# Kernel optimization log

Measured on AMD Instinct MI355X. Metric: run time of the kernel, lower is better.

## Reference

```python
import jax, jax.numpy as jnp
import numpy as np

B, N, P_CTR, K = 16, 2048, 256, 32
H, W = 24, 80
INFEA = 64
MLP = [64, 128, 128, 256]
DIST = 0.5
EPS = 1e-5


def setup_inputs() -> dict:
    key = jax.random.key(0)
    ks = jax.random.split(key, 12)
    inp = {}
    inp['pc'] = jax.random.normal(ks[0], (B, 3, N), jnp.float32)
    inp['feat'] = jax.random.normal(ks[1], (B, INFEA, N), jnp.float32)
    inp['img1'] = jax.random.normal(ks[2], (B, MLP[0], H, W), jnp.float32)
    inp['img2'] = jax.random.normal(ks[3], (B, MLP[1], H, W), jnp.float32)
    inp['P'] = jax.random.normal(ks[4], (B, 3, 4), jnp.float32)
    inp['query_v1'] = jax.random.randint(ks[5], (B, N), 0, H * W, dtype=jnp.int32)
    inp['new_pc'] = jax.random.normal(ks[6], (B, 3, P_CTR), jnp.float32)
    dims = [INFEA + 3] + MLP  # conv chain: 67->64->128->128->256, 1x1 convs, no bias
    for i in range(4):
        fan_in = dims[i]
        inp[f'w{i+1}'] = jax.random.normal(ks[7 + i], (dims[i + 1], dims[i]), jnp.float32) * np.sqrt(2.0 / fan_in)
        inp[f'g{i+1}'] = jnp.ones((dims[i + 1],), jnp.float32)   # BN gamma, init 1
        inp[f'b{i+1}'] = jnp.zeros((dims[i + 1],), jnp.float32)  # BN beta, init 0
    return inp


def query_depth_point(pc, new_pc, dist, k):
    # depth (z-axis) ball query: pc (B,3,N), new_pc (B,3,P) -> idx (B,P,k) int32, num (B,P)
    dz = jnp.abs(pc[:, 2, None, :] - new_pc[:, 2, :, None])  # (B,P,N)
    mask = dz < dist
    num = jnp.sum(mask, axis=-1).astype(jnp.int32)           # neighbor count per center
    # stable argsort of ~mask puts valid indices first, in ascending original order
    order = jnp.argsort(jnp.logical_not(mask), axis=-1, stable=True)
    idx = order[..., :k]
    slot_valid = jnp.arange(k)[None, None, :] < jnp.minimum(num, k)[..., None]
    idx = jnp.where(slot_valid, idx, idx[..., :1])           # pad with first valid index
    return idx.astype(jnp.int32), num


def gather_ch(x, idx):
    # x (B,C,M), idx (B,L) -> (B,C,L)
    return jnp.take_along_axis(x, idx[:, None, :], axis=2)


def conv_bn_relu(x, w, g, b):
    # 1x1 conv (no bias) + BatchNorm2d (training-mode batch stats) + ReLU
    y = jnp.einsum('oc,bcnk->bonk', w, x)
    m = jnp.mean(y, axis=(0, 2, 3), keepdims=True)
    v = jnp.var(y, axis=(0, 2, 3), keepdims=True)
    y = (y - m) * jax.lax.rsqrt(v + EPS)
    y = y * g[None, :, None, None] + b[None, :, None, None]
    return jax.nn.relu(y)


def reference(pc, feat, img1, img2, P, query_v1, new_pc,
              w1, g1, b1, w2, g2, b2, w3, g3, b3, w4, g4, b4):
    idx, num = query_depth_point(pc, new_pc, DIST, K)       # (B,P,K), (B,P)
    idx_flat = idx.reshape(B, P_CTR * K)
    idx_rgb = jnp.take_along_axis(query_v1, idx_flat, axis=1)  # (B,P*K) pixel ids

    grouped_pc = gather_ch(pc, idx_flat).reshape(B, 3, P_CTR, K) - new_pc[:, :, :, None]
    grouped_feat = gather_ch(feat, idx_flat).reshape(B, INFEA, P_CTR, K)
    rgb1 = gather_ch(img1.reshape(B, MLP[0], H * W), idx_rgb).reshape(B, MLP[0], P_CTR, K)
    rgb2 = gather_ch(img2.reshape(B, MLP[1], H * W), idx_rgb).reshape(B, MLP[1], P_CTR, K)

    grouped = jnp.concatenate([grouped_pc, grouped_feat], axis=1)  # (B,67,P,K)
    pf = conv_bn_relu(grouped, w1, g1, b1)                         # (B,64,P,K)
    f1 = jnp.concatenate([pf, rgb1], axis=1)                       # (B,128,P,K)
    pf = conv_bn_relu(pf, w2, g2, b2)                              # (B,128,P,K)
    f2 = jnp.concatenate([pf, rgb2], axis=1)                       # (B,256,P,K)
    pf = conv_bn_relu(pf, w3, g3, b3)
    pf = conv_bn_relu(pf, w4, g4, b4)                              # (B,256,P,K)
    out = jnp.concatenate([f1, f2, pf], axis=1)                    # (B,640,P,K)
    valid = (num > 0).reshape(B, 1, P_CTR, 1).astype(out.dtype)
    return out * valid
```

## Files before the change

kernel.cpp:

```cpp
#include <hip/hip_runtime.h>
#include <hip/hip_fp16.h>

#define BB 16
#define NN 2048
#define PC 256
#define KK 32
#define HWS 1920
#define PT (BB*PC*KK)
#define EPSF 1e-5f
#define THR 512

#define CH_IDXR 256
#define CH_IDX  257
#define CH_VAL  258
#define CH_FT   356
#define STATS_OFF ((size_t)259 << 13)

typedef _Float16 f16x8 __attribute__((ext_vector_type(8)));
typedef float    f32x4 __attribute__((ext_vector_type(4)));

__device__ __forceinline__ unsigned packh2(float lo, float hi) {
  unsigned a = (unsigned)__half_as_ushort(__float2half(lo));
  unsigned b = (unsigned)__half_as_ushort(__float2half(hi));
  return a | (b << 16);
}
__device__ __forceinline__ float h2lo(unsigned u) {
  return __half2float(__ushort_as_half((unsigned short)(u & 0xffffu)));
}
__device__ __forceinline__ float h2hi(unsigned u) {
  return __half2float(__ushort_as_half((unsigned short)(u >> 16)));
}

__global__ __launch_bounds__(256,2) void k_prep(
    const float* __restrict__ feat, float* out)
{
  __shared__ float tile[64][261];
  int tid = threadIdx.x;
  int b = blockIdx.x >> 3, n0 = (blockIdx.x & 7) << 8;
  #pragma unroll 8
  for (int c = 0; c < 64; c++)
    tile[c][tid] = feat[((size_t)b*64 + c)*NN + n0 + tid];
  __syncthreads();
  unsigned* ftw = (unsigned*)out + (((size_t)b*640 + CH_FT)<<13);
  #pragma unroll
  for (int e = tid; e < 256*32; e += 256) {
    int q = e & 31, nl = e >> 5;
    ftw[(size_t)(n0 + nl)*32 + q] = packh2(tile[2*q][nl], tile[2*q+1][nl]);
  }
}

template<bool WSC>
__global__ __launch_bounds__(256) void k_idx(
    const float* __restrict__ pc, const float* __restrict__ npc,
    const int* __restrict__ qv1, float* out, int* __restrict__ wsi)
{
  __shared__ int slots[4][KK];
  int tid = threadIdx.x;
  if (blockIdx.x < 5) {
    int i = blockIdx.x*256 + tid;
    if (i < 1152) out[STATS_OFF + i] = 0.0f;
  }
  int wl = tid >> 6, lane = tid & 63;
  int w = blockIdx.x*4 + wl;
  int b = w >> 8, p = w & 255;
  if (lane == 0) slots[wl][0] = 0;
  float zc = npc[(b*3+2)*PC + p];
  const float* pz = pc + ((size_t)b*3+2)*NN;
  int num = 0;
  for (int ci=0; ci<NN/64; ci++) {
    int n = ci*64 + lane;
    bool m = fabsf(pz[n] - zc) < 0.5f;
    unsigned long long mk = __ballot(m);
    if (m) {
      int rank = num + __popcll(mk & ((1ull<<lane)-1ull));
      if (rank < KK) slots[wl][rank] = n;
    }
    num += __popcll(mk);
  }
  __syncthreads();
  if (lane < KK) {
    int nj = (lane < num) ? slots[wl][lane] : slots[wl][0];
    size_t col = (size_t)p*KK + lane;
    int enc = (num > 0) ? qv1[b*NN + nj] : -1;
    ((int*)out)[(((size_t)b*640 + CH_IDX )<<13) + col] = nj;
    ((int*)out)[(((size_t)b*640 + CH_IDXR)<<13) + col] = enc;
    if constexpr (WSC) wsi[(size_t)b*8192 + col] = enc;
  }
  if (lane == 0)
    out[(((size_t)b*640 + CH_VAL)<<13) + (size_t)p*KK] = (num > 0) ? 1.0f : 0.0f;
}

template<int CIN, int CINP, int COUT, int BOCH, int WVP, int WVO, int WFP, int WFO,
         int XMODE, int XBASE, int YMODE, int YBASE, int STIN, int STOUT,
         int SWZ, int QR, int PFB, int TILES>
__global__ __launch_bounds__(THR,4) void k_mfma(
    const float* __restrict__ pc, const float* __restrict__ npc,
    const float* __restrict__ W,
    const float* __restrict__ g, const float* __restrict__ bv,
    const float* __restrict__ go, const float* __restrict__ bo,
    float* out)
{
  constexpr int KC = CINP/32;
  __shared__ __align__(16) _Float16 xs[2][128*QR*2];
  __shared__ float scs[128], shs[128];
  __shared__ float redu[WVP*BOCH*2];

  int tid = threadIdx.x;
  int tile0 = blockIdx.x * TILES;
  int b = tile0 >> 6;
  int och0 = blockIdx.y * BOCH;

  int wv = tid >> 6, lane = tid & 63;
  int wp = wv % WVP, wo = wv / WVP;
  int lr = lane & 15, lg = lane >> 4;
  int prow0 = wp*(WFP*16), orow0 = wo*(WFO*16);

  f16x8 bfr[KC][WFO];
  #pragma unroll
  for (int kc = 0; kc < KC; kc++)
    #pragma unroll
    for (int fo = 0; fo < WFO; fo++) {
      int orow = och0 + orow0 + fo*16 + lr;
      f16x8 tf;
      if constexpr (XMODE == 0) {
        #pragma unroll
        for (int j = 0; j < 8; j++) {
          int c = kc*32 + lg*8 + j;
          int r = (c < 64) ? c + 3 : (c < 67 ? c - 64 : -1);
          tf[j] = (_Float16)((r >= 0) ? W[(size_t)orow*CIN + r] : 0.f);
        }
      } else {
        const float* wr = W + (size_t)orow*CIN + kc*32 + lg*8;
        float4 w0 = *(const float4*)wr;
        float4 w1 = *(const float4*)(wr + 4);
        tf[0]=(_Float16)w0.x; tf[1]=(_Float16)w0.y; tf[2]=(_Float16)w0.z; tf[3]=(_Float16)w0.w;
        tf[4]=(_Float16)w1.x; tf[5]=(_Float16)w1.y; tf[6]=(_Float16)w1.z; tf[7]=(_Float16)w1.w;
      }
      bfr[kc][fo] = tf;
    }

  if constexpr (XMODE == 1) {
    const float* stin = out + STATS_OFF + STIN;
    for (int c = tid; c < CIN; c += THR) {
      float m   = stin[c] * (1.0f/PT);
      float var = stin[CIN+c]*(1.0f/PT) - m*m;
      float s = rsqrtf(var + EPSF) * g[c];
      scs[c] = s; shs[c] = bv[c] - m*s;
    }
  }
  float osc_[WFO], osh_[WFO];
  if constexpr (YMODE == 3) {
    const float* sto = out + STATS_OFF + STOUT;
    #pragma unroll
    for (int fo = 0; fo < WFO; fo++) {
      int och = och0 + orow0 + fo*16 + lr;
      float m   = sto[och]*(1.0f/PT);
      float var = sto[COUT+och]*(1.0f/PT) - m*m;
      float s = rsqrtf(var + EPSF) * go[och];
      osc_[fo] = s; osh_[fo] = bo[och] - m*s;
    }
  }
  __syncthreads();

  auto STAGE = [&](int t) {
    int col0t = ((tile0 + t) & 63) << 7;
    unsigned* xw = (unsigned*)xs[t & 1];
    if constexpr (XMODE == 0) {
      int posl = tid & 127;
      int qb0  = tid >> 7;
      int n = ((const int*)out)[(((size_t)b*640 + CH_IDX)<<13) + col0t + posl];
      const unsigned* ftw = (const unsigned*)out + (((size_t)b*640 + CH_FT)<<13);
      int pcol = (col0t + posl) >> 5;
      #pragma unroll
      for (int k = 0; k < 12; k++) {
        int q = qb0 + k*4;
        unsigned u;
        if (q < 32) {
          u = ftw[(size_t)n*32 + q];
        } else if (q == 32) {
          float vx = pc[((size_t)b*3+0)*NN + n] - npc[(b*3+0)*PC + pcol];
          float vy = pc[((size_t)b*3+1)*NN + n] - npc[(b*3+1)*PC + pcol];
          u = packh2(vx, vy);
        } else if (q == 33) {
          float vz = pc[((size_t)b*3+2)*NN + n] - npc[(b*3+2)*PC + pcol];
          u = packh2(vz, 0.f);
        } else u = 0u;
        int qs = (((q>>2) ^ ((posl>>2) & SWZ)) << 2) | (q & 3);
        xw[posl*QR + qs] = u;
      }
    } else {
      #pragma unroll
      for (int k = 0; k < CIN/32; k++) {
        int e = tid + k*THR;
        int q = e >> 5, pg = e & 31;
        uint4 u = *(const uint4*)&((const unsigned*)out)[(((size_t)b*640 + XBASE + q)<<13) + col0t + pg*4];
        float s0 = scs[2*q], h0 = shs[2*q], s1 = scs[2*q+1], h1 = shs[2*q+1];
        unsigned uu[4] = {u.x, u.y, u.z, u.w};
        float lo_a[4], hi_a[4];
        #pragma unroll
        for (int j = 0; j < 4; j++) {
          lo_a[j] = fmaxf(fmaf(h2lo(uu[j]), s0, h0), 0.f);
          hi_a[j] = fmaxf(fmaf(h2hi(uu[j]), s1, h1), 0.f);
          int p = pg*4 + j;
          xw[p*QR + ((((q>>2) ^ ((p>>2) & SWZ)) << 2) | (q & 3))] = packh2(lo_a[j], hi_a[j]);
        }
        if constexpr (PFB >= 0) {
          float vv = out[(((size_t)b*640 + CH_VAL)<<13) + col0t + ((pg >> 3) << 5)];
          float4 L  = {lo_a[0]*vv, lo_a[1]*vv, lo_a[2]*vv, lo_a[3]*vv};
          float4 Hh = {hi_a[0]*vv, hi_a[1]*vv, hi_a[2]*vv, hi_a[3]*vv};
          size_t pb = (((size_t)b*640 + PFB + 2*q)<<13) + col0t + pg*4;
          *(float4*)&out[pb]           = L;
          *(float4*)&out[pb + (1<<13)] = Hh;
        }
      }
    }
  };

  STAGE(0);
  __syncthreads();

  float ssum[WFO], ssq[WFO];
  #pragma unroll
  for (int fo = 0; fo < WFO; fo++) { ssum[fo] = 0.f; ssq[fo] = 0.f; }

  #pragma unroll
  for (int t = 0; t < TILES; t++) {
    int col0t = ((tile0 + t) & 63) << 7;
    const _Float16* xb = xs[t & 1];

    f32x4 acc[WFP][WFO];
    const f32x4 zero4 = {0.f, 0.f, 0.f, 0.f};
    #pragma unroll
    for (int fp = 0; fp < WFP; fp++)
      #pragma unroll
      for (int fo = 0; fo < WFO; fo++) acc[fp][fo] = zero4;

    #pragma unroll
    for (int kc = 0; kc < KC; kc++) {
      f16x8 af[WFP];
      #pragma unroll
      for (int fp = 0; fp < WFP; fp++) {
        int row = prow0 + fp*16 + lr;
        int qb = (kc*4 + lg) ^ ((row>>2) & SWZ);
        af[fp] = *(const f16x8*)&xb[row*(QR*2) + qb*8];
      }
      #pragma unroll
      for (int fp = 0; fp < WFP; fp++)
        #pragma unroll
        for (int fo = 0; fo < WFO; fo++)
          acc[fp][fo] = __builtin_amdgcn_mfma_f32_16x16x32_f16(af[fp], bfr[kc][fo], acc[fp][fo], 0, 0, 0);
    }

    if constexpr (YMODE == 1) {
      #pragma unroll
      for (int fp = 0; fp < WFP; fp++) {
        int pos = col0t + prow0 + fp*16 + lg*4;
        #pragma unroll
        for (int fo = 0; fo < WFO; fo++) {
          float pr0 = __shfl_xor(acc[fp][fo][0], 1);
          float pr1 = __shfl_xor(acc[fp][fo][1], 1);
          float pr2 = __shfl_xor(acc[fp][fo][2], 1);
          float pr3 = __shfl_xor(acc[fp][fo][3], 1);
          if (!(lane & 1)) {
            uint4 u;
            u.x = packh2(acc[fp][fo][0], pr0); u.y = packh2(acc[fp][fo][1], pr1);
            u.z = packh2(acc[fp][fo][2], pr2); u.w = packh2(acc[fp][fo][3], pr3);
            int qrow = (och0 + orow0 + fo*16 + lr) >> 1;
            *(uint4*)&((unsigned*)out)[(((size_t)b*640 + YBASE + qrow)<<13) + pos] = u;
          }
        }
      }
    } else if constexpr (YMODE == 3) {
      #pragma unroll
      for (int fp = 0; fp < WFP; fp++) {
        int pos = col0t + prow0 + fp*16 + lg*4;
        float v = out[(((size_t)b*640 + CH_VAL)<<13) + (pos & ~31)];
        #pragma unroll
        for (int fo = 0; fo < WFO; fo++) {
          int och = och0 + orow0 + fo*16 + lr;
          f32x4 wv;
          #pragma unroll
          for (int r = 0; r < 4; r++)
            wv[r] = fmaxf(fmaf(acc[fp][fo][r], osc_[fo], osh_[fo]), 0.f) * v;
          *(f32x4*)&out[(((size_t)b*640 + YBASE + och)<<13) + pos] = wv;
        }
      }
    }

    if constexpr (YMODE != 3) {
      #pragma unroll
      for (int fo = 0; fo < WFO; fo++)
        #pragma unroll
        for (int fp = 0; fp < WFP; fp++)
          #pragma unroll
          for (int r = 0; r < 4; r++) {
            float v = acc[fp][fo][r];
            ssum[fo] += v; ssq[fo] += v*v;
          }
    }

    if (t + 1 < TILES) STAGE(t + 1);
    __syncthreads();
  }

  if constexpr (YMODE != 3) {
    #pragma unroll
    for (int fo = 0; fo < WFO; fo++) {
      float s = ssum[fo], q2 = ssq[fo];
      s  += __shfl_down(s, 32);  s  += __shfl_down(s, 16);
      q2 += __shfl_down(q2, 32); q2 += __shfl_down(q2, 16);
      if (lane < 16) {
        int oloc = orow0 + fo*16 + lane;
        redu[(wp*BOCH + oloc)*2]     = s;
        redu[(wp*BOCH + oloc)*2 + 1] = q2;
      }
    }
    __syncthreads();
    float* stg = out + STATS_OFF + STOUT;
    for (int i = tid; i < BOCH; i += THR) {
      float ss = 0.f, qq = 0.f;
      #pragma unroll
      for (int p = 0; p < WVP; p++) { ss += redu[(p*BOCH + i)*2]; qq += redu[(p*BOCH + i)*2 + 1]; }
      atomicAdd(&stg[och0 + i], ss);
      atomicAdd(&stg[COUT + och0 + i], qq);
    }
  }
}

__global__ __launch_bounds__(512) void k_rgb_lds(
    const float* __restrict__ img1, const float* __restrict__ img2,
    const int* __restrict__ wsi, float* out)
{
  __shared__ float ls[4][HWS];
  int tid = threadIdx.x;
  int b = blockIdx.x / 48, gq = blockIdx.x % 48;
  int gc0 = gq * 4;
  for (int e = tid; e < 4*(HWS/4); e += 512) {
    int c = e / (HWS/4), off = e % (HWS/4);
    int gc = gc0 + c;
    const float* src = (gc < 64) ? img1 + ((size_t)b*64 + gc)*HWS
                                 : img2 + ((size_t)b*128 + (gc-64))*HWS;
    *(float4*)&ls[c][off*4] = *(const float4*)&src[off*4];
  }
  __syncthreads();
  const int* idr = wsi + (size_t)b*8192;
  int dch0 = (gc0 < 64) ? 64 + gc0 : 256 + (gc0 - 64);
  for (int pp = tid; pp < 8192; pp += 512) {
    int enc = idr[pp];
    float v = (enc >= 0) ? 1.0f : 0.0f;
    int ir  = (enc >= 0) ? enc : 0;
    #pragma unroll
    for (int c = 0; c < 4; c++)
      out[(((size_t)b*640 + dch0 + c)<<13) + pp] = ls[c][ir] * v;
  }
}

__global__ __launch_bounds__(256) void k_rgb_fb(
    const float* __restrict__ img1, const float* __restrict__ img2, float* out)
{
  int tid = threadIdx.x;
  int pos = blockIdx.x*256 + tid;
  int b = pos >> 13, rem = pos & 8191;
  int enc = ((const int*)out)[(((size_t)b*640 + CH_IDXR)<<13) + rem];
  float v  = (enc >= 0) ? 1.0f : 0.0f;
  int  ir  = (enc >= 0) ? enc : 0;
  size_t o1 = (((size_t)b*640 + 64)<<13) + rem;
  const float* i1 = img1 + (size_t)b*64*HWS + ir;
  #pragma unroll 8
  for (int c=0;c<64;c++) out[o1 + ((size_t)c<<13)] = i1[(size_t)c*HWS] * v;
  size_t o2 = (((size_t)b*640 + 256)<<13) + rem;
  const float* i2 = img2 + (size_t)b*128*HWS + ir;
  #pragma unroll 8
  for (int c=0;c<128;c++) out[o2 + ((size_t)c<<13)] = i2[(size_t)c*HWS] * v;
}

extern "C" void kernel_launch(void* const* d_in, const int* in_sizes, int n_in,
                              void* d_out, int out_size, void* d_ws, size_t ws_size,
                              hipStream_t stream)
{
  const float* pc   = (const float*)d_in[0];
  const float* feat = (const float*)d_in[1];
  const float* img1 = (const float*)d_in[2];
  const float* img2 = (const float*)d_in[3];
  const int*   qv1  = (const int*)d_in[5];
  const float* npc  = (const float*)d_in[6];
  const float* w1 = (const float*)d_in[7];
  const float* g1 = (const float*)d_in[8];
  const float* b1 = (const float*)d_in[9];
  const float* w2 = (const float*)d_in[10];
  const float* g2 = (const float*)d_in[11];
  const float* b2 = (const float*)d_in[12];
  const float* w3 = (const float*)d_in[13];
  const float* g3 = (const float*)d_in[14];
  const float* b3 = (const float*)d_in[15];
  const float* w4 = (const float*)d_in[16];
  const float* g4 = (const float*)d_in[17];
  const float* b4 = (const float*)d_in[18];
  float* out = (float*)d_out;
  int*  wsi = (int*)d_ws;
  const bool use_ws = (d_ws != nullptr) && (ws_size >= (size_t)BB*8192*4);

  k_prep <<<128,256,0,stream>>>(feat, out);
  if (use_ws) k_idx<true ><<<1024,256,0,stream>>>(pc, npc, qv1, out, wsi);
  else        k_idx<false><<<1024,256,0,stream>>>(pc, npc, qv1, out, wsi);
  k_mfma<67,96,64,64,    2,4,4,1, 0,0,   1,324, 0,0,     0,48, -1,2>
      <<<dim3(512,1),THR,0,stream>>>(pc,npc,w1,g1,b1,g1,b1,out);
  k_mfma<64,64,128,128,  2,4,4,2, 1,324, 1,260, 0,128,   7,36, 0,2>
      <<<dim3(512,1),THR,0,stream>>>(pc,npc,w2,g1,b1,g1,b1,out);
  k_mfma<128,128,128,128,2,4,4,2, 1,260, 1,64,  128,384, 7,68, 128,2>
      <<<dim3(512,1),THR,0,stream>>>(pc,npc,w3,g2,b2,g2,b2,out);
  k_mfma<128,128,256,128,2,4,4,2, 1,64,  2,0,   384,640, 7,68, -1,2>
      <<<dim3(512,2),THR,0,stream>>>(pc,npc,w4,g3,b3,g3,b3,out);
  k_mfma<128,128,256,128,2,4,4,2, 1,64,  3,384, 384,640, 7,68, -1,2>
      <<<dim3(512,2),THR,0,stream>>>(pc,npc,w4,g3,b3,g4,b4,out);
  if (use_ws) k_rgb_lds<<<768,512,0,stream>>>(img1, img2, wsi, out);
  else        k_rgb_fb <<<512,256,0,stream>>>(img1, img2, out);
}
```

Baseline: 579.9 us.

## Shard BN stat atomics across workspace copies and retune MFMA wave layout

BatchNorm sum/sumsq atomics are spread over 32 workspace copies chosen per block, so many blocks no longer contend on the same addresses. Consumers reduce the copies when computing scale/shift, and the final stage stages its output stats in LDS. k_idx now zeroes the extra copies. The wave tiling of the MFMA kernels also changes from 2x4 to 4x2 waves (pos x out), which alters per-wave fragment shapes and register use. The trade-off is extra stat reads per block.

Measured after the change: 748.5 us. 1.29x slower.

```diff
diff --git a/kernel.cpp b/kernel.cpp
--- a/kernel.cpp
+++ b/kernel.cpp
@@ -9,6 +9,7 @@
 #define PT (BB*PC*KK)
 #define EPSF 1e-5f
 #define THR 512
+#define NSTC 32
 
 #define CH_IDXR 256
 #define CH_IDX  257
@@ -52,16 +53,22 @@
 template<bool WSC>
 __global__ __launch_bounds__(256) void k_idx(
     const float* __restrict__ pc, const float* __restrict__ npc,
-    const int* __restrict__ qv1, float* out, int* __restrict__ wsi)
+    const int* __restrict__ qv1, float* out, int* __restrict__ wsi,
+    float* __restrict__ stz)
 {
   __shared__ int slots[4][KK];
   int tid = threadIdx.x;
-  if (blockIdx.x < 5) {
-    int i = blockIdx.x*256 + tid;
+  int bx = blockIdx.x;
+  if (bx < 5) {
+    int i = bx*256 + tid;
     if (i < 1152) out[STATS_OFF + i] = 0.0f;
   }
+  if (stz != nullptr && bx >= 5 && bx < 5 + (NSTC*1152 + 255)/256) {
+    int i = (bx - 5)*256 + tid;
+    if (i < NSTC*1152) stz[i] = 0.0f;
+  }
   int wl = tid >> 6, lane = tid & 63;
-  int w = blockIdx.x*4 + wl;
+  int w = bx*4 + wl;
   int b = w >> 8, p = w & 255;
   if (lane == 0) slots[wl][0] = 0;
   float zc = npc[(b*3+2)*PC + p];
@@ -98,17 +105,19 @@
     const float* __restrict__ W,
     const float* __restrict__ g, const float* __restrict__ bv,
     const float* __restrict__ go, const float* __restrict__ bo,
-    float* out)
+    float* __restrict__ stc, int nc, float* out)
 {
   constexpr int KC = CINP/32;
   __shared__ __align__(16) _Float16 xs[2][128*QR*2];
   __shared__ float scs[128], shs[128];
   __shared__ float redu[WVP*BOCH*2];
+  __shared__ float ost[(YMODE==3) ? 2*BOCH : 1];
 
   int tid = threadIdx.x;
   int tile0 = blockIdx.x * TILES;
   int b = tile0 >> 6;
   int och0 = blockIdx.y * BOCH;
+  int bh = (blockIdx.x + blockIdx.y*7) & (nc - 1);
 
   int wv = tid >> 6, lane = tid & 63;
   int wp = wv % WVP, wo = wv / WVP;
@@ -140,27 +149,38 @@
     }
 
   if constexpr (XMODE == 1) {
-    const float* stin = out + STATS_OFF + STIN;
     for (int c = tid; c < CIN; c += THR) {
-      float m   = stin[c] * (1.0f/PT);
-      float var = stin[CIN+c]*(1.0f/PT) - m*m;
+      float s0 = 0.f, s1 = 0.f;
+      for (int k = 0; k < nc; k++) {
+        s0 += stc[k*1152 + STIN + c];
+        s1 += stc[k*1152 + STIN + CIN + c];
+      }
+      float m   = s0 * (1.0f/PT);
+      float var = s1 * (1.0f/PT) - m*m;
       float s = rsqrtf(var + EPSF) * g[c];
       scs[c] = s; shs[c] = bv[c] - m*s;
     }
   }
+  if constexpr (YMODE == 3) {
+    for (int i = tid; i < 2*BOCH; i += THR) {
+      int gi = STOUT + ((i < BOCH) ? (och0 + i) : (COUT + och0 + (i - BOCH)));
+      float s = 0.f;
+      for (int k = 0; k < nc; k++) s += stc[k*1152 + gi];
+      ost[i] = s;
+    }
+  }
+  __syncthreads();
   float osc_[WFO], osh_[WFO];
   if constexpr (YMODE == 3) {
-    const float* sto = out + STATS_OFF + STOUT;
     #pragma unroll
     for (int fo = 0; fo < WFO; fo++) {
-      int och = och0 + orow0 + fo*16 + lr;
-      float m   = sto[och]*(1.0f/PT);
-      float var = sto[COUT+och]*(1.0f/PT) - m*m;
-      float s = rsqrtf(var + EPSF) * go[och];
-      osc_[fo] = s; osh_[fo] = bo[och] - m*s;
-    }
-  }
-  __syncthreads();
+      int oloc = orow0 + fo*16 + lr;
+      float m   = ost[oloc]*(1.0f/PT);
+      float var = ost[BOCH+oloc]*(1.0f/PT) - m*m;
+      float s = rsqrtf(var + EPSF) * go[och0 + oloc];
+      osc_[fo] = s; osh_[fo] = bo[och0 + oloc] - m*s;
+    }
+  }
 
   auto STAGE = [&](int t) {
     int col0t = ((tile0 + t) & 63) << 7;
@@ -278,11 +298,11 @@
         #pragma unroll
         for (int fo = 0; fo < WFO; fo++) {
           int och = och0 + orow0 + fo*16 + lr;
-          f32x4 wv;
+          f32x4 wvv;
           #pragma unroll
           for (int r = 0; r < 4; r++)
-            wv[r] = fmaxf(fmaf(acc[fp][fo][r], osc_[fo], osh_[fo]), 0.f) * v;
-          *(f32x4*)&out[(((size_t)b*640 + YBASE + och)<<13) + pos] = wv;
+            wvv[r] = fmaxf(fmaf(acc[fp][fo][r], osc_[fo], osh_[fo]), 0.f) * v;
+          *(f32x4*)&out[(((size_t)b*640 + YBASE + och)<<13) + pos] = wvv;
         }
       }
     }
@@ -316,7 +336,7 @@
       }
     }
     __syncthreads();
-    float* stg = out + STATS_OFF + STOUT;
+    float* stg = stc + (size_t)bh*1152 + STOUT;
     for (int i = tid; i < BOCH; i += THR) {
       float ss = 0.f, qq = 0.f;
       #pragma unroll
@@ -399,20 +419,23 @@
   float* out = (float*)d_out;
   int*  wsi = (int*)d_ws;
   const bool use_ws = (d_ws != nullptr) && (ws_size >= (size_t)BB*8192*4);
+  const bool use_st = (d_ws != nullptr) && (ws_size >= (size_t)BB*8192*4 + (size_t)NSTC*1152*4);
+  float* stc = use_st ? ((float*)d_ws + BB*8192) : (out + STATS_OFF);
+  int    nc  = use_st ? NSTC : 1;
 
   k_prep <<<128,256,0,stream>>>(feat, out);
-  if (use_ws) k_idx<true ><<<1024,256,0,stream>>>(pc, npc, qv1, out, wsi);
-  else        k_idx<false><<<1024,256,0,stream>>>(pc, npc, qv1, out, wsi);
-  k_mfma<67,96,64,64,    2,4,4,1, 0,0,   1,324, 0,0,     0,48, -1,2>
-      <<<dim3(512,1),THR,0,stream>>>(pc,npc,w1,g1,b1,g1,b1,out);
-  k_mfma<64,64,128,128,  2,4,4,2, 1,324, 1,260, 0,128,   7,36, 0,2>
-      <<<dim3(512,1),THR,0,stream>>>(pc,npc,w2,g1,b1,g1,b1,out);
-  k_mfma<128,128,128,128,2,4,4,2, 1,260, 1,64,  128,384, 7,68, 128,2>
-      <<<dim3(512,1),THR,0,stream>>>(pc,npc,w3,g2,b2,g2,b2,out);
-  k_mfma<128,128,256,128,2,4,4,2, 1,64,  2,0,   384,640, 7,68, -1,2>
-      <<<dim3(512,2),THR,0,stream>>>(pc,npc,w4,g3,b3,g3,b3,out);
-  k_mfma<128,128,256,128,2,4,4,2, 1,64,  3,384, 384,640, 7,68, -1,2>
-      <<<dim3(512,2),THR,0,stream>>>(pc,npc,w4,g3,b3,g4,b4,out);
+  if (use_ws) k_idx<true ><<<1024,256,0,stream>>>(pc, npc, qv1, out, wsi, use_st ? stc : nullptr);
+  else        k_idx<false><<<1024,256,0,stream>>>(pc, npc, qv1, out, wsi, use_st ? stc : nullptr);
+  k_mfma<67,96,64,64,    4,2,2,2, 0,0,   1,324, 0,0,     0,48, -1,2>
+      <<<dim3(512,1),THR,0,stream>>>(pc,npc,w1,g1,b1,g1,b1,stc,nc,out);
+  k_mfma<64,64,128,128,  4,2,2,4, 1,324, 1,260, 0,128,   7,36, 0,2>
+      <<<dim3(512,1),THR,0,stream>>>(pc,npc,w2,g1,b1,g1,b1,stc,nc,out);
+  k_mfma<128,128,128,128,4,2,2,4, 1,260, 1,64,  128,384, 7,68, 128,2>
+      <<<dim3(512,1),THR,0,stream>>>(pc,npc,w3,g2,b2,g2,b2,stc,nc,out);
+  k_mfma<128,128,256,128,4,2,2,4, 1,64,  2,0,   384,640, 7,68, -1,2>
+      <<<dim3(512,2),THR,0,stream>>>(pc,npc,w4,g3,b3,g3,b3,stc,nc,out);
+  k_mfma<128,128,256,128,4,2,2,4, 1,64,  3,384, 384,640, 7,68, -1,2>
+      <<<dim3(512,2),THR,0,stream>>>(pc,npc,w4,g3,b3,g4,b4,stc,nc,out);
   if (use_ws) k_rgb_lds<<<768,512,0,stream>>>(img1, img2, wsi, out);
   else        k_rgb_fb <<<512,256,0,stream>>>(img1, img2, out);
 }
```
